# Kernel optimization log

Hardware: AMD Instinct MI355X
Metric: run time of the kernel (lower is better)

## Reference

```python
import jax, jax.numpy as jnp
import numpy as np

PAD_VALUE = -1e10  # matches torch F.pad(value=-1e10); padded cells are sliced away before output


def setup_inputs() -> dict:
    key = jax.random.key(0)
    x = jax.random.normal(key, (8, 16, 256, 256), dtype=jnp.float32)
    return {"x": x, "d": 5}


def reference(x, d):
    # x: (B, C, H, W). Builds a shift-graph: each pixel connects to the d*d-1
    # pixels in a d x d window; weight = -||f1-f2||^2 * sqrt(di^2+dj^2).
    B, C, H, W = x.shape
    r = d // 2
    id0 = jnp.arange(H * W, dtype=jnp.int32).reshape(H, W)
    img_pad = jnp.pad(x, ((0, 0), (0, 0), (r, r), (r, r)), constant_values=PAD_VALUE)
    ws, edges = [], []
    for i in range(d):
        for j in range(d):
            if i == r and j == r:
                continue
            pos_v = (i - r) * W + (j - r)
            # shifted view of the padded image, aligned with x: (B, C, H, W)
            f1 = img_pad[:, :, i:H + i, j:W + j]
            scale = float(((i - r) ** 2 + (j - r) ** 2) ** 0.5)
            dist = -((f1 - x) ** 2).sum(axis=1) * scale  # (B, H, W)
            # crop to the region where the shifted neighbor is in-bounds
            h0, h1 = max(r - i, 0), H - max(i - r, 0)
            w0, w1 = max(r - j, 0), W - max(j - r, 0)
            imgx = dist[:, h0:h1, w0:w1].reshape(B, -1)  # (B, n_ij)
            idx = id0[h0:h1, w0:w1].reshape(-1)          # (n_ij,)
            pos = jnp.broadcast_to(idx[None, :], (B, idx.shape[0]))
            ws.append(imgx)
            edges.append(jnp.stack((pos, pos + pos_v), axis=-1))  # (B, n_ij, 2)
    return jnp.concatenate(edges, axis=-2), jnp.concatenate(ws, axis=-1)
```

## Files before the change

### kernel.cpp

```cpp
#include <hip/hip_runtime.h>


#define HH 256
#define WW 256
#define CC 16
#define BB 8
#define HW (HH * WW)
#define EE 1557540

__global__ __launch_bounds__(256) void shiftgraph_kernel(
    const float* __restrict__ x, float* __restrict__ out) {
    __shared__ float lds[3080];
    const int bid = blockIdx.x;
    const int b = bid & 7;
    const int h = bid >> 3;
    const int w = threadIdx.x;

    const float* __restrict__ xb = x + (size_t)b * (CC * HW);

    const float* src[3];
    int dst[3];
#pragma unroll
    for (int inst = 0; inst < 3; ++inst) {
        const int flatf = inst * 1024 + w * 4;
        const int cl  = flatf / 768;
        const int rem = flatf - cl * 768;
        const int row = rem >> 8;
        const int col = rem & 255;
        int hr = h + row; hr = hr > HH - 1 ? HH - 1 : hr;
        src[inst] = xb + cl * HW + hr * WW + col;
        dst[inst] = flatf;
    }

    float acc[12];
#pragma unroll
    for (int s2 = 0; s2 < 12; ++s2) acc[s2] = 0.0f;

    for (int cc = 0; cc < 4; ++cc) {
        __syncthreads();
#pragma unroll
        for (int inst = 0; inst < 3; ++inst) {
            const float4 v = *reinterpret_cast<const float4*>(src[inst]);
            *reinterpret_cast<float4*>(&lds[dst[inst]]) = v;
            src[inst] += 4 * HW;
        }
        __syncthreads();
#pragma unroll
        for (int c = 0; c < 4; ++c) {
            const int base = c * 768 + w;
            const float ctr = lds[base];
            float d;
            d = lds[base + 1] - ctr; acc[0] = fmaf(d, d, acc[0]);
            d = lds[base + 2] - ctr; acc[1] = fmaf(d, d, acc[1]);
#pragma unroll
            for (int dj = -2; dj <= 2; ++dj) {
                d = lds[base + 256 + dj] - ctr;
                acc[4 + dj] = fmaf(d, d, acc[4 + dj]);
                d = lds[base + 512 + dj] - ctr;
                acc[9 + dj] = fmaf(d, d, acc[9 + dj]);
            }
        }
    }

    float* __restrict__ edges = out;
    float* __restrict__ wsp   = out + (size_t)BB * EE * 2;
    const size_t bE = (size_t)b * EE;
    const int posc = h * WW + w;

    int s = 0;
#pragma unroll
    for (int di = 0; di <= 2; ++di) {
#pragma unroll
        for (int dj = (di == 0 ? 1 : -2); dj <= 2; ++dj, ++s) {
            const int i = di + 2, j = dj + 2;
            if (h + di >= HH) continue;
            const int w2 = w + dj;
            if (w2 < 0 || w2 >= WW) continue;

            const float scale = sqrtf((float)(di * di + dj * dj));
            const float wsv = -acc[s] * scale;

            int offF = 0, offM = 0;
#pragma unroll
            for (int m = 0; m < 25; ++m) {
                const int mi = m / 5, mj = m % 5;
                if (mi == 2 && mj == 2) continue;
                const int cm = (HH - (mi < 2 ? 2 - mi : mi - 2)) *
                               (WW - (mj < 2 ? 2 - mj : mj - 2));
                if (m < i * 5 + j) offF += cm;
                if (m < (4 - i) * 5 + (4 - j)) offM += cm;
            }
            const int cww = WW - (dj < 0 ? -dj : dj);
            const int e1 = offF + h * cww + (w - (dj < 0 ? -dj : 0));
            const int e2 = offM + h * cww + (w + (dj < 0 ? dj : 0));
            const int posv = di * WW + dj;

            *reinterpret_cast<float2*>(edges + (bE + e1) * 2) =
                make_float2((float)posc, (float)(posc + posv));
            *reinterpret_cast<float2*>(edges + (bE + e2) * 2) =
                make_float2((float)(posc + posv), (float)posc);
            wsp[bE + e1] = wsv;
            wsp[bE + e2] = wsv;
        }
    }
}

extern "C" void kernel_launch(void* const* d_in, const int* in_sizes, int n_in,
                              void* d_out, int out_size, void* d_ws, size_t ws_size,
                              hipStream_t stream) {
    const float* x = (const float*)d_in[0];
    float* out = (float*)d_out;
    dim3 block(WW);
    dim3 grid(HH * BB);
    shiftgraph_kernel<<<grid, block, 0, stream>>>(x, out);
}
```

Before: 33.64 us.

## Give each wavefront a private LDS slice with halo and prefetch channels

Each 64-lane wavefront now stages its own 72-column halo tile per channel group in a private LDS slice, so the block-wide __syncthreads barriers are removed. The next channel group's global loads are issued into registers before the current group is computed, then written into LDS afterwards. This overlaps memory latency with compute and avoids block-wide stalls. The cost is redundant halo loads at the wavefront edges and higher register use. Because the same slice is overwritten with no barrier at all, correctness depends on the wavefront executing in lockstep.

```diff
diff --git a/kernel.cpp b/kernel.cpp
--- a/kernel.cpp
+++ b/kernel.cpp
@@ -10,54 +10,84 @@
 
 __global__ __launch_bounds__(256) void shiftgraph_kernel(
     const float* __restrict__ x, float* __restrict__ out) {
-    __shared__ float lds[3080];
+    __shared__ float lds[4][872];
     const int bid = blockIdx.x;
     const int b = bid & 7;
     const int h = bid >> 3;
-    const int w = threadIdx.x;
+    const int tid = threadIdx.x;
+    const int wv = tid >> 6;
+    const int lane = tid & 63;
+    const int w0 = wv << 6;
+    const int w = tid;
 
     const float* __restrict__ xb = x + (size_t)b * (CC * HW);
+    float* __restrict__ slice = lds[wv];
 
-    const float* src[3];
-    int dst[3];
+    const float* src[4];
+    int dst[4];
+    bool act[4];
 #pragma unroll
-    for (int inst = 0; inst < 3; ++inst) {
-        const int flatf = inst * 1024 + w * 4;
-        const int cl  = flatf / 768;
-        const int rem = flatf - cl * 768;
-        const int row = rem >> 8;
-        const int col = rem & 255;
+    for (int inst = 0; inst < 4; ++inst) {
+        const int g = lane + inst * 64;
+        act[inst] = (g < 216);
+        const int gg = act[inst] ? g : 215;
+        const int F = gg * 4;
+        const int ch  = F / 216;
+        const int rem = F - ch * 216;
+        const int row = rem / 72;
+        const int colofs = rem - row * 72;
+        int c0 = w0 - 4 + colofs;
+        c0 = c0 < 0 ? 0 : (c0 > 252 ? 252 : c0);
         int hr = h + row; hr = hr > HH - 1 ? HH - 1 : hr;
-        src[inst] = xb + cl * HW + hr * WW + col;
-        dst[inst] = flatf;
+        src[inst] = xb + ch * HW + hr * WW + c0;
+        dst[inst] = F;
+    }
+
+#pragma unroll
+    for (int inst = 0; inst < 4; ++inst) {
+        if (act[inst]) {
+            *reinterpret_cast<float4*>(&slice[dst[inst]]) =
+                *reinterpret_cast<const float4*>(src[inst]);
+            src[inst] += 4 * HW;
+        }
     }
 
     float acc[12];
 #pragma unroll
     for (int s2 = 0; s2 < 12; ++s2) acc[s2] = 0.0f;
 
+#pragma unroll
     for (int cc = 0; cc < 4; ++cc) {
-        __syncthreads();
+        float4 pf[4];
+        if (cc < 3) {
 #pragma unroll
-        for (int inst = 0; inst < 3; ++inst) {
-            const float4 v = *reinterpret_cast<const float4*>(src[inst]);
-            *reinterpret_cast<float4*>(&lds[dst[inst]]) = v;
-            src[inst] += 4 * HW;
+            for (int inst = 0; inst < 4; ++inst) {
+                if (act[inst]) {
+                    pf[inst] = *reinterpret_cast<const float4*>(src[inst]);
+                    src[inst] += 4 * HW;
+                }
+            }
         }
-        __syncthreads();
 #pragma unroll
         for (int c = 0; c < 4; ++c) {
-            const int base = c * 768 + w;
-            const float ctr = lds[base];
+            const int base = c * 216 + lane + 4;
+            const float ctr = slice[base];
             float d;
-            d = lds[base + 1] - ctr; acc[0] = fmaf(d, d, acc[0]);
-            d = lds[base + 2] - ctr; acc[1] = fmaf(d, d, acc[1]);
+            d = slice[base + 1] - ctr; acc[0] = fmaf(d, d, acc[0]);
+            d = slice[base + 2] - ctr; acc[1] = fmaf(d, d, acc[1]);
 #pragma unroll
             for (int dj = -2; dj <= 2; ++dj) {
-                d = lds[base + 256 + dj] - ctr;
+                d = slice[base + 72 + dj] - ctr;
                 acc[4 + dj] = fmaf(d, d, acc[4 + dj]);
-                d = lds[base + 512 + dj] - ctr;
+                d = slice[base + 144 + dj] - ctr;
                 acc[9 + dj] = fmaf(d, d, acc[9 + dj]);
+            }
+        }
+        if (cc < 3) {
+#pragma unroll
+            for (int inst = 0; inst < 4; ++inst) {
+                if (act[inst])
+                    *reinterpret_cast<float4*>(&slice[dst[inst]]) = pf[inst];
             }
         }
     }
@@ -110,7 +140,7 @@
                               hipStream_t stream) {
     const float* x = (const float*)d_in[0];
     float* out = (float*)d_out;
-    dim3 block(WW);
+    dim3 block(256);
     dim3 grid(HH * BB);
     shiftgraph_kernel<<<grid, block, 0, stream>>>(x, out);
 }
```

Result: slower. 48.12 us (+43.0%).

## Interleave edge-index stores with channel loads and use lightweight barriers

Applied to the files above, without the earlier changes.

Edge-index pair stores, which depend only on position, are spread across the four channel-chunk iterations (three offsets per iteration), so their global writes overlap with the loads and LDS compute of later chunks instead of all landing at the end. The __syncthreads calls are replaced by raw s_barrier plus sched_barrier with an explicit lgkmcnt wait, and the first barrier is skipped. This aims to hide output write traffic behind input loading and cut barrier overhead. The risks are higher register pressure and more instruction scheduling constraints from the full unroll.

```diff
diff --git a/kernel.cpp b/kernel.cpp
--- a/kernel.cpp
+++ b/kernel.cpp
@@ -32,19 +32,32 @@
         dst[inst] = flatf;
     }
 
+    float* __restrict__ edges = out;
+    float* __restrict__ wsp   = out + (size_t)BB * EE * 2;
+    const size_t bE = (size_t)b * EE;
+    const int posc = h * WW + w;
+
     float acc[12];
 #pragma unroll
     for (int s2 = 0; s2 < 12; ++s2) acc[s2] = 0.0f;
 
+#pragma unroll
     for (int cc = 0; cc < 4; ++cc) {
-        __syncthreads();
+        if (cc > 0) {
+            asm volatile("" ::: "memory");
+            __builtin_amdgcn_s_barrier();
+            __builtin_amdgcn_sched_barrier(0);
+        }
 #pragma unroll
         for (int inst = 0; inst < 3; ++inst) {
             const float4 v = *reinterpret_cast<const float4*>(src[inst]);
             *reinterpret_cast<float4*>(&lds[dst[inst]]) = v;
             src[inst] += 4 * HW;
         }
-        __syncthreads();
+        asm volatile("s_waitcnt lgkmcnt(0)" ::: "memory");
+        __builtin_amdgcn_s_barrier();
+        __builtin_amdgcn_sched_barrier(0);
+
 #pragma unroll
         for (int c = 0; c < 4; ++c) {
             const int base = c * 768 + w;
@@ -60,12 +73,42 @@
                 acc[9 + dj] = fmaf(d, d, acc[9 + dj]);
             }
         }
+
+        {
+            int s = 0;
+#pragma unroll
+            for (int di = 0; di <= 2; ++di) {
+#pragma unroll
+                for (int dj = (di == 0 ? 1 : -2); dj <= 2; ++dj, ++s) {
+                    if (s < cc * 3 || s >= cc * 3 + 3) continue;
+                    const int i = di + 2, j = dj + 2;
+                    if (h + di >= HH) continue;
+                    const int w2 = w + dj;
+                    if (w2 < 0 || w2 >= WW) continue;
+
+                    int offF = 0, offM = 0;
+#pragma unroll
+                    for (int m = 0; m < 25; ++m) {
+                        const int mi = m / 5, mj = m % 5;
+                        if (mi == 2 && mj == 2) continue;
+                        const int cm = (HH - (mi < 2 ? 2 - mi : mi - 2)) *
+                                       (WW - (mj < 2 ? 2 - mj : mj - 2));
+                        if (m < i * 5 + j) offF += cm;
+                        if (m < (4 - i) * 5 + (4 - j)) offM += cm;
+                    }
+                    const int cww = WW - (dj < 0 ? -dj : dj);
+                    const int e1 = offF + h * cww + (w - (dj < 0 ? -dj : 0));
+                    const int e2 = offM + h * cww + (w + (dj < 0 ? dj : 0));
+                    const int posv = di * WW + dj;
+
+                    *reinterpret_cast<float2*>(edges + (bE + e1) * 2) =
+                        make_float2((float)posc, (float)(posc + posv));
+                    *reinterpret_cast<float2*>(edges + (bE + e2) * 2) =
+                        make_float2((float)(posc + posv), (float)posc);
+                }
+            }
+        }
     }
-
-    float* __restrict__ edges = out;
-    float* __restrict__ wsp   = out + (size_t)BB * EE * 2;
-    const size_t bE = (size_t)b * EE;
-    const int posc = h * WW + w;
 
     int s = 0;
 #pragma unroll
@@ -93,12 +136,7 @@
             const int cww = WW - (dj < 0 ? -dj : dj);
             const int e1 = offF + h * cww + (w - (dj < 0 ? -dj : 0));
             const int e2 = offM + h * cww + (w + (dj < 0 ? dj : 0));
-            const int posv = di * WW + dj;
 
-            *reinterpret_cast<float2*>(edges + (bE + e1) * 2) =
-                make_float2((float)posc, (float)(posc + posv));
-            *reinterpret_cast<float2*>(edges + (bE + e2) * 2) =
-                make_float2((float)(posc + posv), (float)posc);
             wsp[bE + e1] = wsv;
             wsp[bE + e2] = wsv;
         }
```

After: 32.91 us, median of 2. 2.2% less time.

## Process two output rows per block and load all channels to LDS at once

Applied to the files above, without the earlier changes.

Each block now handles two image rows with 512 threads and stages all 16 channels of four input rows into 64KB of LDS in a single pass, instead of looping over four channel chunks with two barriers each. This cuts the number of redundant halo-row loads per output row from three to two, and each thread keeps its center pixel values in registers. The distance is then computed per neighbor direction, right before its stores. The larger LDS footprint limits how many blocks fit per CU and may reduce occupancy.

```diff
diff --git a/kernel.cpp b/kernel.cpp
--- a/kernel.cpp
+++ b/kernel.cpp
@@ -8,99 +8,85 @@
 #define HW (HH * WW)
 #define EE 1557540
 
-__global__ __launch_bounds__(256) void shiftgraph_kernel(
+__global__ __launch_bounds__(512) void shiftgraph_kernel(
     const float* __restrict__ x, float* __restrict__ out) {
-    __shared__ float lds[3080];
+    __shared__ float lds[16384];
     const int bid = blockIdx.x;
-    const int b = bid & 7;
-    const int h = bid >> 3;
-    const int w = threadIdx.x;
+    const int b  = bid & 7;
+    const int hg = bid >> 3;
+    const int tid = threadIdx.x;
+    const int rr = tid >> 8;
+    const int w  = tid & 255;
+    const int h  = hg * 2 + rr;
 
     const float* __restrict__ xb = x + (size_t)b * (CC * HW);
 
-    const float* src[3];
-    int dst[3];
 #pragma unroll
-    for (int inst = 0; inst < 3; ++inst) {
-        const int flatf = inst * 1024 + w * 4;
-        const int cl  = flatf / 768;
-        const int rem = flatf - cl * 768;
+    for (int inst = 0; inst < 8; ++inst) {
+        const int flatf = inst * 2048 + tid * 4;
+        const int ch  = flatf >> 10;
+        const int rem = flatf & 1023;
         const int row = rem >> 8;
         const int col = rem & 255;
-        int hr = h + row; hr = hr > HH - 1 ? HH - 1 : hr;
-        src[inst] = xb + cl * HW + hr * WW + col;
-        dst[inst] = flatf;
+        int hr = hg * 2 + row; hr = hr > HH - 1 ? HH - 1 : hr;
+        *reinterpret_cast<float4*>(&lds[flatf]) =
+            *reinterpret_cast<const float4*>(xb + ch * HW + hr * WW + col);
     }
+    __syncthreads();
 
-    float acc[12];
+    float ctr[CC];
 #pragma unroll
-    for (int s2 = 0; s2 < 12; ++s2) acc[s2] = 0.0f;
-
-    for (int cc = 0; cc < 4; ++cc) {
-        __syncthreads();
-#pragma unroll
-        for (int inst = 0; inst < 3; ++inst) {
-            const float4 v = *reinterpret_cast<const float4*>(src[inst]);
-            *reinterpret_cast<float4*>(&lds[dst[inst]]) = v;
-            src[inst] += 4 * HW;
-        }
-        __syncthreads();
-#pragma unroll
-        for (int c = 0; c < 4; ++c) {
-            const int base = c * 768 + w;
-            const float ctr = lds[base];
-            float d;
-            d = lds[base + 1] - ctr; acc[0] = fmaf(d, d, acc[0]);
-            d = lds[base + 2] - ctr; acc[1] = fmaf(d, d, acc[1]);
-#pragma unroll
-            for (int dj = -2; dj <= 2; ++dj) {
-                d = lds[base + 256 + dj] - ctr;
-                acc[4 + dj] = fmaf(d, d, acc[4 + dj]);
-                d = lds[base + 512 + dj] - ctr;
-                acc[9 + dj] = fmaf(d, d, acc[9 + dj]);
-            }
-        }
-    }
+    for (int c = 0; c < CC; ++c) ctr[c] = lds[c * 1024 + rr * 256 + w];
 
     float* __restrict__ edges = out;
     float* __restrict__ wsp   = out + (size_t)BB * EE * 2;
     const size_t bE = (size_t)b * EE;
     const int posc = h * WW + w;
 
-    int s = 0;
 #pragma unroll
     for (int di = 0; di <= 2; ++di) {
 #pragma unroll
-        for (int dj = (di == 0 ? 1 : -2); dj <= 2; ++dj, ++s) {
+        for (int dj = (di == 0 ? 1 : -2); dj <= 2; ++dj) {
             const int i = di + 2, j = dj + 2;
             if (h + di >= HH) continue;
             const int w2 = w + dj;
-            if (w2 < 0 || w2 >= WW) continue;
+            const bool wok = (w2 >= 0 && w2 < WW);
+            int wn = w + dj; wn = wn < 0 ? 0 : (wn > WW - 1 ? WW - 1 : wn);
+            const int nbase = (rr + di) * 256 + wn;
 
-            const float scale = sqrtf((float)(di * di + dj * dj));
-            const float wsv = -acc[s] * scale;
+            float acc = 0.0f;
+#pragma unroll
+            for (int c = 0; c < CC; ++c) {
+                const float d = lds[c * 1024 + nbase] - ctr[c];
+                acc = fmaf(d, d, acc);
+            }
 
-            int offF = 0, offM = 0;
+            if (wok) {
+                const float scale = sqrtf((float)(di * di + dj * dj));
+                const float wsv = -acc * scale;
+
+                int offF = 0, offM = 0;
 #pragma unroll
-            for (int m = 0; m < 25; ++m) {
-                const int mi = m / 5, mj = m % 5;
-                if (mi == 2 && mj == 2) continue;
-                const int cm = (HH - (mi < 2 ? 2 - mi : mi - 2)) *
-                               (WW - (mj < 2 ? 2 - mj : mj - 2));
-                if (m < i * 5 + j) offF += cm;
-                if (m < (4 - i) * 5 + (4 - j)) offM += cm;
+                for (int m = 0; m < 25; ++m) {
+                    const int mi = m / 5, mj = m % 5;
+                    if (mi == 2 && mj == 2) continue;
+                    const int cm = (HH - (mi < 2 ? 2 - mi : mi - 2)) *
+                                   (WW - (mj < 2 ? 2 - mj : mj - 2));
+                    if (m < i * 5 + j) offF += cm;
+                    if (m < (4 - i) * 5 + (4 - j)) offM += cm;
+                }
+                const int cww = WW - (dj < 0 ? -dj : dj);
+                const int e1 = offF + h * cww + (w - (dj < 0 ? -dj : 0));
+                const int e2 = offM + h * cww + (w + (dj < 0 ? dj : 0));
+                const int posv = di * WW + dj;
+
+                *reinterpret_cast<float2*>(edges + (bE + e1) * 2) =
+                    make_float2((float)posc, (float)(posc + posv));
+                *reinterpret_cast<float2*>(edges + (bE + e2) * 2) =
+                    make_float2((float)(posc + posv), (float)posc);
+                wsp[bE + e1] = wsv;
+                wsp[bE + e2] = wsv;
             }
-            const int cww = WW - (dj < 0 ? -dj : dj);
-            const int e1 = offF + h * cww + (w - (dj < 0 ? -dj : 0));
-            const int e2 = offM + h * cww + (w + (dj < 0 ? dj : 0));
-            const int posv = di * WW + dj;
-
-            *reinterpret_cast<float2*>(edges + (bE + e1) * 2) =
-                make_float2((float)posc, (float)(posc + posv));
-            *reinterpret_cast<float2*>(edges + (bE + e2) * 2) =
-                make_float2((float)(posc + posv), (float)posc);
-            wsp[bE + e1] = wsv;
-            wsp[bE + e2] = wsv;
         }
     }
 }
@@ -110,7 +96,7 @@
                               hipStream_t stream) {
     const float* x = (const float*)d_in[0];
     float* out = (float*)d_out;
-    dim3 block(WW);
-    dim3 grid(HH * BB);
+    dim3 block(512);
+    dim3 grid(128 * BB);
     shiftgraph_kernel<<<grid, block, 0, stream>>>(x, out);
 }
```

Result: no change. 33.29 us (-1.0%).
